# Optimization experiments

Hardware: AMD Instinct MI355X
Metric: run time of the kernel (lower is better)

Reference implementation:

```python
import jax, jax.numpy as jnp
import numpy as np

BANDWIDTH = 512.0


def _pairwise_lse(A, B, bandwidth):
    """logsumexp over all pairs of exp(-||a-b||^2 / bandwidth).

    Matches torch: vmap over rows b of B computing logsumexp over A,
    then logsumexp over those row results == single logsumexp over the
    full [Na, Nb] matrix of -sq_dist/bandwidth.
    """
    # squared distances via ||a||^2 + ||b||^2 - 2 a.b  (GEMM-dominated)
    a2 = jnp.sum(A * A, axis=-1)  # [Na]
    b2 = jnp.sum(B * B, axis=-1)  # [Nb]
    d2 = a2[:, None] + b2[None, :] - 2.0 * (A @ B.T)  # [Na, Nb]
    return jax.nn.logsumexp(-d2 / bandwidth)


def setup_inputs() -> dict:
    key = jax.random.key(0)
    kx, ky = jax.random.split(key)
    X = jax.random.normal(kx, (8192, 512), dtype=jnp.float32)
    Y = jax.random.normal(ky, (8192, 512), dtype=jnp.float32)
    return {"X": X, "Y": Y}


def reference(X, Y):
    n = X.shape[0]
    m = Y.shape[0]
    xx = (jnp.exp(_pairwise_lse(X, X, BANDWIDTH)) - n) / (n * (n - 1))
    xy = jnp.exp(_pairwise_lse(X, Y, BANDWIDTH)) / (n * m)
    yy = (jnp.exp(_pairwise_lse(Y, Y, BANDWIDTH)) - m) / (m * (m - 1))
    return xx - 2.0 * xy + yy
```

## Files before the change

kernel.cpp:

```cpp
#include <hip/hip_runtime.h>
#include <math.h>


#define D      512
#define BTM    128
#define BTN    256
#define BK     16
#define KSTEPS (D / BK)

#define AHI 0
#define ALO 256
#define BHI 512
#define BLO 1024

typedef _Float16 half8 __attribute__((ext_vector_type(8)));
typedef __attribute__((ext_vector_type(8)))  short  short8;
typedef __attribute__((ext_vector_type(16))) float  f32x16;

union U4H8 { uint4 u; half8 h; };
union U4S8 { uint4 u; short8 s; };

__device__ __forceinline__ unsigned short bf16_rne(float x) {
    unsigned u = __float_as_uint(x);
    return (unsigned short)((u + 0x7fffu + ((u >> 16) & 1u)) >> 16);
}
__device__ __forceinline__ float bf16_f32(unsigned short b) {
    return __uint_as_float(((unsigned)b) << 16);
}
__device__ __forceinline__ void split8(const float v[8], uint4& hi, uint4& lo) {
    unsigned h[8], l[8];
    #pragma unroll
    for (int j = 0; j < 8; j++) {
        unsigned short bh = bf16_rne(v[j]);
        float r = v[j] - bf16_f32(bh);
        unsigned short bl = bf16_rne(r);
        h[j] = bh; l[j] = bl;
    }
    hi.x = h[0] | (h[1] << 16); hi.y = h[2] | (h[3] << 16);
    hi.z = h[4] | (h[5] << 16); hi.w = h[6] | (h[7] << 16);
    lo.x = l[0] | (l[1] << 16); lo.y = l[2] | (l[3] << 16);
    lo.z = l[4] | (l[5] << 16); lo.w = l[6] | (l[7] << 16);
}

__device__ __forceinline__ void lds16(const uint4* g, uint4* l) {
    __builtin_amdgcn_global_load_lds(
        (const __attribute__((address_space(1))) void*)g,
        (__attribute__((address_space(3))) void*)(unsigned int)(uintptr_t)(void*)l,
        16, 0, 0);
}

__global__ void init_kernel(double* accum, unsigned* minkey) {
    if (threadIdx.x < 3) accum[threadIdx.x] = 0.0;
    if (threadIdx.x < 4) minkey[threadIdx.x] = 0xFFFFFFFFu;
}

__global__ __launch_bounds__(256)
void convert_h_kernel(const float* __restrict__ X, const float* __restrict__ Y,
                      uint4* __restrict__ Xh, uint4* __restrict__ Yh, int npts) {
    const float* src = blockIdx.z ? Y : X;
    uint4*       dst = blockIdx.z ? Yh : Xh;
    const int ks = blockIdx.y;
    const int p  = blockIdx.x * 256 + threadIdx.x;
    if (p >= npts) return;
    const float* s = src + (size_t)p * D + ks * BK;
    float v[16];
    *(float4*)&v[0]  = *(const float4*)(s);
    *(float4*)&v[4]  = *(const float4*)(s + 4);
    *(float4*)&v[8]  = *(const float4*)(s + 8);
    *(float4*)&v[12] = *(const float4*)(s + 12);
    U4H8 a, b;
    #pragma unroll
    for (int j = 0; j < 8; j++) { a.h[j] = (_Float16)v[j]; b.h[j] = (_Float16)v[8 + j]; }
    size_t u = (size_t)ks * npts * 2 + (size_t)(p >> 5) * 64 + (p & 31);
    dst[u] = a.u; dst[u + 32] = b.u;
}

__global__ __launch_bounds__(256)
void row_norms_kernel(const float* __restrict__ X, const float* __restrict__ Y,
                      float* __restrict__ X2, float* __restrict__ Y2, int N, int M) {
    const int wave = threadIdx.x >> 6;
    const int lane = threadIdx.x & 63;
    const int row  = blockIdx.x * 4 + wave;
    const float* src; float* dst; int r;
    if (row < N)          { src = X; dst = X2; r = row; }
    else if (row < N + M) { src = Y; dst = Y2; r = row - N; }
    else return;
    const float* p = src + (size_t)r * D;
    float s = 0.f;
    #pragma unroll
    for (int c = 0; c < D; c += 64) {
        float v = p[c + lane];
        s = fmaf(v, v, s);
    }
    #pragma unroll
    for (int off = 32; off > 0; off >>= 1) s += __shfl_down(s, off);
    if (lane == 0) dst[r] = s;
}

__device__ inline unsigned float_key(float f) {
    unsigned u = __float_as_uint(f);
    return (u & 0x80000000u) ? ~u : (u | 0x80000000u);
}
__device__ inline float key_float(unsigned k) {
    return __uint_as_float((k & 0x80000000u) ? (k ^ 0x80000000u) : ~k);
}

__global__ __launch_bounds__(256)
void diag_min_bits_kernel(const float* __restrict__ X, const float* __restrict__ Y,
                          const float* __restrict__ X2, const float* __restrict__ Y2,
                          unsigned* __restrict__ minkey, int ngx) {
    int b = blockIdx.x;
    const float *src, *n2; int zidx;
    if (b < ngx) { src = X; n2 = X2; zidx = 0; }
    else         { src = Y; n2 = Y2; zidx = 2; b -= ngx; }

    const int tid  = threadIdx.x;
    const int wave = tid >> 6, lane = tid & 63;
    const int grp  = b * 4 + wave;
    const int fp   = lane & 31, fh = lane >> 5;
    const int pt   = grp * 32 + fp;
    const float* s = src + (size_t)pt * D + fh * 8;

    f32x16 acc;
    #pragma unroll
    for (int i = 0; i < 16; i++) acc[i] = 0.f;

    for (int ks = 0; ks < KSTEPS; ks++) {
        float v[8];
        *(float4*)&v[0] = *(const float4*)(s + ks * BK);
        *(float4*)&v[4] = *(const float4*)(s + ks * BK + 4);
        U4S8 hi, lo;
        split8(v, hi.u, lo.u);
        short8 ah = hi.s, al = lo.s;
        acc = __builtin_amdgcn_mfma_f32_32x32x16_bf16(ah, ah, acc, 0, 0, 0);
        acc = __builtin_amdgcn_mfma_f32_32x32x16_bf16(ah, al, acc, 0, 0, 0);
        acc = __builtin_amdgcn_mfma_f32_32x32x16_bf16(al, ah, acc, 0, 0, 0);
    }

    float dmin = 1e30f;
    if (fh == ((fp >> 2) & 1)) {
        int r = (fp & 3) + 4 * (fp >> 3);
        float av = acc[r];
        float rn = n2[pt];
        float cn = rn;
        float d2 = rn + cn - 2.0f * av;
        dmin = d2;
    }
    #pragma unroll
    for (int off = 32; off > 0; off >>= 1) dmin = fminf(dmin, __shfl_down(dmin, off));
    __shared__ float wm[4];
    __shared__ int   wz[4];
    if (lane == 0) { wm[wave] = dmin; wz[wave] = zidx; }
    __syncthreads();
    if (tid == 0)
        atomicMin(&minkey[wz[0]],
                  float_key(fminf(fminf(wm[0], wm[1]), fminf(wm[2], wm[3]))));
}

__global__ __launch_bounds__(256, 2)
void pair_exp_sum_kernel(const uint4* __restrict__ Xh, const uint4* __restrict__ Yh,
                         const float* __restrict__ X2, const float* __restrict__ Y2,
                         double* __restrict__ accum, float* __restrict__ bmin,
                         int N, int M) {
    const int z = blockIdx.z;
    const uint4 *Ah, *Bh; const float *An, *Bn; bool sym; int na, nb;
    if (z == 0)      { Ah = Xh; Bh = Xh; An = X2; Bn = X2; sym = true;  na = N; nb = N; }
    else if (z == 1) { Ah = Xh; Bh = Yh; An = X2; Bn = Y2; sym = false; na = N; nb = M; }
    else             { Ah = Yh; Bh = Yh; An = Y2; Bn = Y2; sym = true;  na = M; nb = M; }
    const int bi = blockIdx.x, bj = blockIdx.y;
    if (sym && (2 * bj + 1) < bi) return;

    __shared__ uint4  smem[2][1024];
    __shared__ float  smN[BTM + BTN];
    __shared__ double wsum[4];
    __shared__ float  wmin[4];

    const int tid  = threadIdx.x;
    const int wave = tid >> 6, lane = tid & 63;
    const int wy = wave >> 1, wx = wave & 1;
    const int row0 = bi * BTM, col0 = bj * BTN;

    if (tid < BTM) smN[tid] = An[row0 + tid];
    smN[BTM + tid] = Bn[col0 + tid];

    const int wl = wave * 64 + lane;
    const size_t strideA = (size_t)na * 2;
    const size_t strideB = (size_t)nb * 2;
    const uint4* gB0 = Bh + (size_t)(col0 >> 5) * 64 + wl;
    const uint4* gB1 = gB0 + 256;
    const half8* gA0 = (const half8*)Ah + ((size_t)(row0 >> 5) + 2 * wy) * 64 + lane;
    const half8* gA1 = gA0 + 64;

    f32x16 acc[2][4];
    #pragma unroll
    for (int g = 0; g < 2; g++)
        #pragma unroll
        for (int c = 0; c < 4; c++)
            #pragma unroll
            for (int i = 0; i < 16; i++) acc[g][c][i] = 0.f;

    auto stage2 = [&](int buf, int ks) {
        lds16(gB0 + (size_t)ks * strideB,       &smem[buf][wl]);
        lds16(gB1 + (size_t)ks * strideB,       &smem[buf][256 + wl]);
        lds16(gB0 + (size_t)(ks + 1) * strideB, &smem[buf][512 + wl]);
        lds16(gB1 + (size_t)(ks + 1) * strideB, &smem[buf][768 + wl]);
    };
    half8 Af[4][2];
    auto loadA2 = [&](int ks, int s) {
        Af[s][0]     = gA0[(size_t)ks * strideA];
        Af[s][1]     = gA1[(size_t)ks * strideA];
        Af[s + 1][0] = gA0[(size_t)(ks + 1) * strideA];
        Af[s + 1][1] = gA1[(size_t)(ks + 1) * strideA];
    };
    auto computeK = [&](const uint4* base, int slot) {
        const half8* p = (const half8*)base;
        half8 bh[4];
        #pragma unroll
        for (int c = 0; c < 4; c++) bh[c] = p[(4 * wx + c) * 64 + lane];
        #pragma unroll
        for (int g = 0; g < 2; g++)
            #pragma unroll
            for (int c = 0; c < 4; c++)
                acc[g][c] = __builtin_amdgcn_mfma_f32_32x32x16_f16(Af[slot][g], bh[c], acc[g][c], 0, 0, 0);
    };

    stage2(0, 0);
    loadA2(0, 0);
    __syncthreads();

    #pragma unroll
    for (int it = 1; it < KSTEPS / 2; it++) {
        stage2(it & 1, 2 * it);
        loadA2(2 * it, (it & 1) * 2);
        computeK(&smem[(it - 1) & 1][0],   ((it - 1) & 1) * 2);
        computeK(&smem[(it - 1) & 1][512], ((it - 1) & 1) * 2 + 1);
        __syncthreads();
    }
    computeK(&smem[1][0],   2);
    computeK(&smem[1][512], 3);

    float wgt = 1.f;
    if (sym) {
        int cblk = 2 * bj + wx;
        wgt = (cblk > bi) ? 2.f : (cblk == bi ? 1.f : 0.f);
    }

    const int fp = lane & 31, fh = lane >> 5;
    double s = 0.0;
    float dmin = 1e30f;
    if (wgt != 0.f) {
        const float* rowN = &smN[64 * wy];
        const float* colN = &smN[BTM + 128 * wx];
        const float kC = -0.0028177637517362567f;
        #pragma unroll
        for (int g = 0; g < 2; g++)
            #pragma unroll
            for (int c = 0; c < 4; c++) {
                float cn = colN[32 * c + fp];
                float rs = 0.f;
                #pragma unroll
                for (int r = 0; r < 16; r++) {
                    int r32 = (r & 3) + 8 * (r >> 2) + 4 * fh;
                    float d2 = rowN[32 * g + r32] + cn - 2.0f * acc[g][c][r];
                    dmin = fminf(dmin, d2);
                    rs += exp2f(d2 * kC);
                }
                s += (double)rs;
            }
        s *= (double)wgt;
    }

    #pragma unroll
    for (int off = 32; off > 0; off >>= 1) {
        s += __shfl_down(s, off);
        dmin = fminf(dmin, __shfl_down(dmin, off));
    }
    if (lane == 0) { wsum[wave] = s; wmin[wave] = dmin; }
    __syncthreads();
    if (tid == 0) {
        atomicAdd(&accum[z], wsum[0] + wsum[1] + wsum[2] + wsum[3]);
        if (z == 1)
            bmin[bi * gridDim.y + bj] = fminf(fminf(wmin[0], wmin[1]),
                                              fminf(wmin[2], wmin[3]));
    }
}

__global__ __launch_bounds__(256)
void xy_gmin_kernel(const float* __restrict__ bmin, float* __restrict__ gmin, int nblk) {
    float m = 1e30f;
    for (int i = threadIdx.x; i < nblk; i += 256) m = fminf(m, bmin[i]);
    #pragma unroll
    for (int off = 32; off > 0; off >>= 1) m = fminf(m, __shfl_down(m, off));
    __shared__ float wm[4];
    if ((threadIdx.x & 63) == 0) wm[threadIdx.x >> 6] = m;
    __syncthreads();
    if (threadIdx.x == 0) gmin[0] = fminf(fminf(wm[0], wm[1]), fminf(wm[2], wm[3]));
}

__global__ __launch_bounds__(256)
void refine_min_kernel(const float* __restrict__ A, const float* __restrict__ B,
                       const float* __restrict__ An, const float* __restrict__ Bn,
                       const float* __restrict__ bmin, const float* __restrict__ gmin,
                       unsigned* __restrict__ minkey, int zidx) {
    const int bi = blockIdx.x;
    const int bj = blockIdx.y;
    if (!(bmin[bi * gridDim.y + bj] < gmin[0] + 0.5f)) return;
    const int row0 = bi * BTM, col0 = bj * BTN;

    __shared__ uint4 smem[1536];
    __shared__ float smN[BTM + BTN];
    __shared__ float wmin[4];

    const int tid  = threadIdx.x;
    const int wave = tid >> 6, lane = tid & 63;
    const int wy = wave >> 1, wx = wave & 1;
    if (tid < BTM) smN[tid] = An[row0 + tid];
    smN[BTM + tid] = Bn[col0 + tid];

    const int fp = lane & 31, fh = lane >> 5;
    int au[2], bu[4];
    #pragma unroll
    for (int g = 0; g < 2; g++) au[g] = (64 * wy + 32 * g + fp) * 2 + fh;
    #pragma unroll
    for (int c = 0; c < 4; c++) bu[c] = (128 * wx + 32 * c + fp) * 2 + fh;

    f32x16 acc[2][4];
    #pragma unroll
    for (int g = 0; g < 2; g++)
        #pragma unroll
        for (int c = 0; c < 4; c++)
            #pragma unroll
            for (int i = 0; i < 16; i++) acc[g][c][i] = 0.f;

    for (int ks = 0; ks < KSTEPS; ks++) {
        __syncthreads();
        {
            const float* s = A + (size_t)(row0 + (tid >> 1)) * D + ks * BK + (tid & 1) * 8;
            float v[8];
            *(float4*)&v[0] = *(const float4*)s;
            *(float4*)&v[4] = *(const float4*)(s + 4);
            uint4 hi, lo; split8(v, hi, lo);
            smem[AHI + tid] = hi; smem[ALO + tid] = lo;
        }
        #pragma unroll
        for (int t = 0; t < 2; t++) {
            int u = tid + t * 256;
            const float* s = B + (size_t)(col0 + (u >> 1)) * D + ks * BK + (u & 1) * 8;
            float v[8];
            *(float4*)&v[0] = *(const float4*)s;
            *(float4*)&v[4] = *(const float4*)(s + 4);
            uint4 hi, lo; split8(v, hi, lo);
            smem[BHI + u] = hi; smem[BLO + u] = lo;
        }
        __syncthreads();
        {
            const short8* p = (const short8*)&smem[0];
            short8 ah[2], al[2], bh[4], bl[4];
            #pragma unroll
            for (int g = 0; g < 2; g++) { ah[g] = p[AHI + au[g]]; al[g] = p[ALO + au[g]]; }
            #pragma unroll
            for (int c = 0; c < 4; c++) { bh[c] = p[BHI + bu[c]]; bl[c] = p[BLO + bu[c]]; }
            #pragma unroll
            for (int g = 0; g < 2; g++)
                #pragma unroll
                for (int c = 0; c < 4; c++)
                    acc[g][c] = __builtin_amdgcn_mfma_f32_32x32x16_bf16(ah[g], bh[c], acc[g][c], 0, 0, 0);
            #pragma unroll
            for (int g = 0; g < 2; g++)
                #pragma unroll
                for (int c = 0; c < 4; c++)
                    acc[g][c] = __builtin_amdgcn_mfma_f32_32x32x16_bf16(ah[g], bl[c], acc[g][c], 0, 0, 0);
            #pragma unroll
            for (int g = 0; g < 2; g++)
                #pragma unroll
                for (int c = 0; c < 4; c++)
                    acc[g][c] = __builtin_amdgcn_mfma_f32_32x32x16_bf16(al[g], bh[c], acc[g][c], 0, 0, 0);
        }
    }

    float dmin = 1e30f;
    const float* rowN = &smN[64 * wy];
    const float* colN = &smN[BTM + 128 * wx];
    #pragma unroll
    for (int g = 0; g < 2; g++)
        #pragma unroll
        for (int c = 0; c < 4; c++) {
            float cn = colN[32 * c + fp];
            #pragma unroll
            for (int r = 0; r < 16; r++) {
                int r32 = (r & 3) + 8 * (r >> 2) + 4 * fh;
                float d2 = rowN[32 * g + r32] + cn - 2.0f * acc[g][c][r];
                dmin = fminf(dmin, d2);
            }
        }

    #pragma unroll
    for (int off = 32; off > 0; off >>= 1) dmin = fminf(dmin, __shfl_down(dmin, off));
    if (lane == 0) wmin[wave] = dmin;
    __syncthreads();
    if (tid == 0)
        atomicMin(&minkey[zidx],
                  float_key(fminf(fminf(wmin[0], wmin[1]), fminf(wmin[2], wmin[3]))));
}

__global__ void finalize_kernel(const double* __restrict__ accum,
                                const unsigned* __restrict__ minkey,
                                float* __restrict__ out, int N, int M) {
    if (threadIdx.x == 0 && blockIdx.x == 0) {
        float Sp[3];
        #pragma unroll
        for (int z = 0; z < 3; z++) {
            float m = key_float(minkey[z]) * (-1.0f / 512.0f);
            double Sshift = accum[z] * exp(-(double)m);
            float r = (float)log(Sshift);
            float lse = r + m;
            Sp[z] = (float)exp((double)lse);
        }
        float nf  = (float)N, mf = (float)M;
        float nn1 = (float)((double)N * (double)(N - 1));
        float mm1 = (float)((double)M * (double)(M - 1));
        float nm  = (float)((double)N * (double)M);
        float xx = (Sp[0] - nf) / nn1;
        float xy =  Sp[1]       / nm;
        float yy = (Sp[2] - mf) / mm1;
        out[0] = xx - 2.0f * xy + yy;
    }
}

extern "C" void kernel_launch(void* const* d_in, const int* in_sizes, int n_in,
                              void* d_out, int out_size, void* d_ws, size_t ws_size,
                              hipStream_t stream) {
    const float* X = (const float*)d_in[0];
    const float* Y = (const float*)d_in[1];
    const int N = in_sizes[0] / D;
    const int M = in_sizes[1] / D;
    const int gx = N / BTM, gy = M / BTN;

    double*   accum  = (double*)d_ws;
    unsigned* minkey = (unsigned*)((char*)d_ws + 32);
    float*    gmin   = (float*)((char*)d_ws + 48);
    float*    X2     = (float*)((char*)d_ws + 64);
    float*    Y2     = X2 + N;
    float*    bmin   = Y2 + M;
    size_t off = (64 + (size_t)(N + M) * 4 + (size_t)gx * gy * 4 + 255) & ~(size_t)255;
    size_t asz = (size_t)N * D * 2;
    uint4* Xh = (uint4*)((char*)d_ws + off);
    uint4* Yh = (uint4*)((char*)d_ws + off + asz);

    init_kernel<<<1, 64, 0, stream>>>(accum, minkey);

    row_norms_kernel<<<(N + M + 3) / 4, 256, 0, stream>>>(X, Y, X2, Y2, N, M);
    convert_h_kernel<<<dim3((N + 255) / 256, KSTEPS, 2), 256, 0, stream>>>(X, Y, Xh, Yh, N);

    diag_min_bits_kernel<<<N / 128 + M / 128, 256, 0, stream>>>(X, Y, X2, Y2, minkey, N / 128);

    dim3 grid(gx, gy, 3);
    pair_exp_sum_kernel<<<grid, 256, 0, stream>>>(Xh, Yh, X2, Y2, accum, bmin, N, M);

    xy_gmin_kernel<<<1, 256, 0, stream>>>(bmin, gmin, gx * gy);
    refine_min_kernel<<<dim3(gx, gy), 256, 0, stream>>>(X, Y, X2, Y2, bmin, gmin,
                                                        minkey, 1);

    finalize_kernel<<<1, 64, 0, stream>>>(accum, minkey, (float*)d_out, N, M);
}
```

Measured before the change: 324.8 us.

## Deepen main GEMM K-staging to four steps and widen refine kernel to 1024 threads

The main pairwise kernel now stages four K-slices of B into LDS per iteration instead of two, with eight register slots for A, so there are half as many barriers and more loads in flight. This doubles LDS use per block to 64 KB and raises register pressure, which may lower occupancy under the 2-blocks-per-SM launch bound. The refine_min kernel is split across 16 waves, each computing a 32x64 subtile, instead of 4 waves each computing 64x128. That spreads the few surviving refine tiles over more waves to cut their latency.

Result: faster. 311.1 us (-4.2%).

```diff
diff --git a/kernel.cpp b/kernel.cpp
--- a/kernel.cpp
+++ b/kernel.cpp
@@ -170,7 +170,7 @@
     const int bi = blockIdx.x, bj = blockIdx.y;
     if (sym && (2 * bj + 1) < bi) return;
 
-    __shared__ uint4  smem[2][1024];
+    __shared__ uint4  smem[2][2048];
     __shared__ float  smN[BTM + BTN];
     __shared__ double wsum[4];
     __shared__ float  wmin[4];
@@ -199,18 +199,20 @@
             #pragma unroll
             for (int i = 0; i < 16; i++) acc[g][c][i] = 0.f;
 
-    auto stage2 = [&](int buf, int ks) {
-        lds16(gB0 + (size_t)ks * strideB,       &smem[buf][wl]);
-        lds16(gB1 + (size_t)ks * strideB,       &smem[buf][256 + wl]);
-        lds16(gB0 + (size_t)(ks + 1) * strideB, &smem[buf][512 + wl]);
-        lds16(gB1 + (size_t)(ks + 1) * strideB, &smem[buf][768 + wl]);
+    auto stage4 = [&](int buf, int ks) {
+        #pragma unroll
+        for (int j = 0; j < 4; j++) {
+            lds16(gB0 + (size_t)(ks + j) * strideB, &smem[buf][j * 512 + wl]);
+            lds16(gB1 + (size_t)(ks + j) * strideB, &smem[buf][j * 512 + 256 + wl]);
+        }
     };
-    half8 Af[4][2];
-    auto loadA2 = [&](int ks, int s) {
-        Af[s][0]     = gA0[(size_t)ks * strideA];
-        Af[s][1]     = gA1[(size_t)ks * strideA];
-        Af[s + 1][0] = gA0[(size_t)(ks + 1) * strideA];
-        Af[s + 1][1] = gA1[(size_t)(ks + 1) * strideA];
+    half8 Af[8][2];
+    auto loadA4 = [&](int ks, int s) {
+        #pragma unroll
+        for (int j = 0; j < 4; j++) {
+            Af[s + j][0] = gA0[(size_t)(ks + j) * strideA];
+            Af[s + j][1] = gA1[(size_t)(ks + j) * strideA];
+        }
     };
     auto computeK = [&](const uint4* base, int slot) {
         const half8* p = (const half8*)base;
@@ -224,20 +226,25 @@
                 acc[g][c] = __builtin_amdgcn_mfma_f32_32x32x16_f16(Af[slot][g], bh[c], acc[g][c], 0, 0, 0);
     };
 
-    stage2(0, 0);
-    loadA2(0, 0);
+    stage4(0, 0);
+    loadA4(0, 0);
     __syncthreads();
 
     #pragma unroll
-    for (int it = 1; it < KSTEPS / 2; it++) {
-        stage2(it & 1, 2 * it);
-        loadA2(2 * it, (it & 1) * 2);
-        computeK(&smem[(it - 1) & 1][0],   ((it - 1) & 1) * 2);
-        computeK(&smem[(it - 1) & 1][512], ((it - 1) & 1) * 2 + 1);
+    for (int it = 1; it < KSTEPS / 4; it++) {
+        stage4(it & 1, 4 * it);
+        loadA4(4 * it, (it & 1) * 4);
+        const int pb = (it - 1) & 1, ps = pb * 4;
+        computeK(&smem[pb][0],    ps + 0);
+        computeK(&smem[pb][512],  ps + 1);
+        computeK(&smem[pb][1024], ps + 2);
+        computeK(&smem[pb][1536], ps + 3);
         __syncthreads();
     }
-    computeK(&smem[1][0],   2);
-    computeK(&smem[1][512], 3);
+    computeK(&smem[1][0],    4);
+    computeK(&smem[1][512],  5);
+    computeK(&smem[1][1024], 6);
+    computeK(&smem[1][1536], 7);
 
     float wgt = 1.f;
     if (sym) {
@@ -297,7 +304,7 @@
     if (threadIdx.x == 0) gmin[0] = fminf(fminf(wm[0], wm[1]), fminf(wm[2], wm[3]));
 }
 
-__global__ __launch_bounds__(256)
+__global__ __launch_bounds__(1024)
 void refine_min_kernel(const float* __restrict__ A, const float* __restrict__ B,
                        const float* __restrict__ An, const float* __restrict__ Bn,
                        const float* __restrict__ bmin, const float* __restrict__ gmin,
@@ -309,42 +316,37 @@
 
     __shared__ uint4 smem[1536];
     __shared__ float smN[BTM + BTN];
-    __shared__ float wmin[4];
+    __shared__ float wmin[16];
 
     const int tid  = threadIdx.x;
     const int wave = tid >> 6, lane = tid & 63;
-    const int wy = wave >> 1, wx = wave & 1;
+    const int gy = wave & 3, cg0 = 2 * (wave >> 2);
     if (tid < BTM) smN[tid] = An[row0 + tid];
-    smN[BTM + tid] = Bn[col0 + tid];
+    if (tid < BTN) smN[BTM + tid] = Bn[col0 + tid];
 
     const int fp = lane & 31, fh = lane >> 5;
-    int au[2], bu[4];
-    #pragma unroll
-    for (int g = 0; g < 2; g++) au[g] = (64 * wy + 32 * g + fp) * 2 + fh;
-    #pragma unroll
-    for (int c = 0; c < 4; c++) bu[c] = (128 * wx + 32 * c + fp) * 2 + fh;
-
-    f32x16 acc[2][4];
-    #pragma unroll
-    for (int g = 0; g < 2; g++)
-        #pragma unroll
-        for (int c = 0; c < 4; c++)
-            #pragma unroll
-            for (int i = 0; i < 16; i++) acc[g][c][i] = 0.f;
+    const int au = (32 * gy + fp) * 2 + fh;
+    int bu[2];
+    #pragma unroll
+    for (int c = 0; c < 2; c++) bu[c] = (32 * (cg0 + c) + fp) * 2 + fh;
+
+    f32x16 acc[2];
+    #pragma unroll
+    for (int c = 0; c < 2; c++)
+        #pragma unroll
+        for (int i = 0; i < 16; i++) acc[c][i] = 0.f;
 
     for (int ks = 0; ks < KSTEPS; ks++) {
         __syncthreads();
-        {
+        if (tid < 256) {
             const float* s = A + (size_t)(row0 + (tid >> 1)) * D + ks * BK + (tid & 1) * 8;
             float v[8];
             *(float4*)&v[0] = *(const float4*)s;
             *(float4*)&v[4] = *(const float4*)(s + 4);
             uint4 hi, lo; split8(v, hi, lo);
             smem[AHI + tid] = hi; smem[ALO + tid] = lo;
-        }
-        #pragma unroll
-        for (int t = 0; t < 2; t++) {
-            int u = tid + t * 256;
+        } else if (tid < 768) {
+            int u = tid - 256;
             const float* s = B + (size_t)(col0 + (u >> 1)) * D + ks * BK + (u & 1) * 8;
             float v[8];
             *(float4*)&v[0] = *(const float4*)s;
@@ -355,52 +357,45 @@
         __syncthreads();
         {
             const short8* p = (const short8*)&smem[0];
-            short8 ah[2], al[2], bh[4], bl[4];
-            #pragma unroll
-            for (int g = 0; g < 2; g++) { ah[g] = p[AHI + au[g]]; al[g] = p[ALO + au[g]]; }
-            #pragma unroll
-            for (int c = 0; c < 4; c++) { bh[c] = p[BHI + bu[c]]; bl[c] = p[BLO + bu[c]]; }
-            #pragma unroll
-            for (int g = 0; g < 2; g++)
-                #pragma unroll
-                for (int c = 0; c < 4; c++)
-                    acc[g][c] = __builtin_amdgcn_mfma_f32_32x32x16_bf16(ah[g], bh[c], acc[g][c], 0, 0, 0);
-            #pragma unroll
-            for (int g = 0; g < 2; g++)
-                #pragma unroll
-                for (int c = 0; c < 4; c++)
-                    acc[g][c] = __builtin_amdgcn_mfma_f32_32x32x16_bf16(ah[g], bl[c], acc[g][c], 0, 0, 0);
-            #pragma unroll
-            for (int g = 0; g < 2; g++)
-                #pragma unroll
-                for (int c = 0; c < 4; c++)
-                    acc[g][c] = __builtin_amdgcn_mfma_f32_32x32x16_bf16(al[g], bh[c], acc[g][c], 0, 0, 0);
+            short8 ah = p[AHI + au], al = p[ALO + au];
+            short8 bh[2], bl[2];
+            #pragma unroll
+            for (int c = 0; c < 2; c++) { bh[c] = p[BHI + bu[c]]; bl[c] = p[BLO + bu[c]]; }
+            #pragma unroll
+            for (int c = 0; c < 2; c++)
+                acc[c] = __builtin_amdgcn_mfma_f32_32x32x16_bf16(ah, bh[c], acc[c], 0, 0, 0);
+            #pragma unroll
+            for (int c = 0; c < 2; c++)
+                acc[c] = __builtin_amdgcn_mfma_f32_32x32x16_bf16(ah, bl[c], acc[c], 0, 0, 0);
+            #pragma unroll
+            for (int c = 0; c < 2; c++)
+                acc[c] = __builtin_amdgcn_mfma_f32_32x32x16_bf16(al, bh[c], acc[c], 0, 0, 0);
         }
     }
 
     float dmin = 1e30f;
-    const float* rowN = &smN[64 * wy];
-    const float* colN = &smN[BTM + 128 * wx];
-    #pragma unroll
-    for (int g = 0; g < 2; g++)
-        #pragma unroll
-        for (int c = 0; c < 4; c++) {
-            float cn = colN[32 * c + fp];
-            #pragma unroll
-            for (int r = 0; r < 16; r++) {
-                int r32 = (r & 3) + 8 * (r >> 2) + 4 * fh;
-                float d2 = rowN[32 * g + r32] + cn - 2.0f * acc[g][c][r];
-                dmin = fminf(dmin, d2);
-            }
-        }
+    const float* rowN = &smN[32 * gy];
+    #pragma unroll
+    for (int c = 0; c < 2; c++) {
+        float cn = smN[BTM + 32 * (cg0 + c) + fp];
+        #pragma unroll
+        for (int r = 0; r < 16; r++) {
+            int r32 = (r & 3) + 8 * (r >> 2) + 4 * fh;
+            float d2 = rowN[r32] + cn - 2.0f * acc[c][r];
+            dmin = fminf(dmin, d2);
+        }
+    }
 
     #pragma unroll
     for (int off = 32; off > 0; off >>= 1) dmin = fminf(dmin, __shfl_down(dmin, off));
     if (lane == 0) wmin[wave] = dmin;
     __syncthreads();
-    if (tid == 0)
-        atomicMin(&minkey[zidx],
-                  float_key(fminf(fminf(wmin[0], wmin[1]), fminf(wmin[2], wmin[3]))));
+    if (tid == 0) {
+        float m = wmin[0];
+        #pragma unroll
+        for (int w = 1; w < 16; w++) m = fminf(m, wmin[w]);
+        atomicMin(&minkey[zidx], float_key(m));
+    }
 }
 
 __global__ void finalize_kernel(const double* __restrict__ accum,
@@ -458,8 +453,8 @@
     pair_exp_sum_kernel<<<grid, 256, 0, stream>>>(Xh, Yh, X2, Y2, accum, bmin, N, M);
 
     xy_gmin_kernel<<<1, 256, 0, stream>>>(bmin, gmin, gx * gy);
-    refine_min_kernel<<<dim3(gx, gy), 256, 0, stream>>>(X, Y, X2, Y2, bmin, gmin,
-                                                        minkey, 1);
+    refine_min_kernel<<<dim3(gx, gy), 1024, 0, stream>>>(X, Y, X2, Y2, bmin, gmin,
+                                                         minkey, 1);
 
     finalize_kernel<<<1, 64, 0, stream>>>(accum, minkey, (float*)d_out, N, M);
 }
```
